# Optimization experiments

Measured on AMD Instinct MI355X. Metric: run time of the kernel, lower is better.

The kernel has to match this reference:

```python
import jax, jax.numpy as jnp
import numpy as np

EPS_GIN = 0.0      # GINConv eps (train_eps=False)
EPS_LN = 1e-5      # LayerNorm eps
EPS_GN = 1e-5      # GraphNorm eps


def _layer_norm(h, w, b):
    mu = jnp.mean(h, axis=-1, keepdims=True)
    var = jnp.mean(jnp.square(h - mu), axis=-1, keepdims=True)
    return (h - mu) * jax.lax.rsqrt(var + EPS_LN) * w + b


def setup_inputs() -> dict:
    key = jax.random.key(0)
    ks = jax.random.split(key, 6)
    N, E, C = 50000, 800000, 64
    x = jax.random.normal(ks[0], (N, C), dtype=jnp.float32)
    edge_index = jax.random.randint(ks[1], (2, E), 0, N, dtype=jnp.int64)
    W0 = jax.random.normal(ks[2], (C, C), dtype=jnp.float32) / np.sqrt(C)
    W1 = jax.random.normal(ks[3], (C, C), dtype=jnp.float32) / np.sqrt(C)
    ln0_w = jnp.ones((C,), jnp.float32); ln0_b = jnp.zeros((C,), jnp.float32)
    ln1_w = jnp.ones((C,), jnp.float32); ln1_b = jnp.zeros((C,), jnp.float32)
    # GraphNorm params
    gn_w = jnp.ones((C,), jnp.float32)
    gn_b = jnp.zeros((C,), jnp.float32)
    gn_alpha = jnp.ones((C,), jnp.float32)  # mean_scale
    return {"x": x, "edge_index": edge_index, "W0": W0, "ln0_w": ln0_w,
            "ln0_b": ln0_b, "W1": W1, "ln1_w": ln1_w, "ln1_b": ln1_b,
            "gn_w": gn_w, "gn_b": gn_b, "gn_alpha": gn_alpha}


def reference(x, edge_index, W0, ln0_w, ln0_b, W1, ln1_w, ln1_b, gn_w, gn_b, gn_alpha):
    N = x.shape[0]
    src, dst = edge_index[0], edge_index[1]
    # GINConv aggregation: sum of source-node features at each target node
    agg = jax.ops.segment_sum(x[src], dst, num_segments=N)  # [N, C]
    h = (1.0 + EPS_GIN) * x + agg
    # MLP: (Linear no-bias -> LayerNorm -> ReLU) x 2
    h = jax.nn.relu(_layer_norm(h @ W0.T, ln0_w, ln0_b))
    h = jax.nn.relu(_layer_norm(h @ W1.T, ln1_w, ln1_b))
    # GraphNorm over the single graph (all nodes)
    mean = jnp.mean(h, axis=0, keepdims=True)                # [1, C]
    out = h - gn_alpha * mean
    var = jnp.mean(jnp.square(out), axis=0, keepdims=True)   # [1, C]
    return gn_w * out * jax.lax.rsqrt(var + EPS_GN) + gn_b
```

## Files before the change

### kernel.cpp

```cpp
#include <hip/hip_runtime.h>
#include <hip/hip_fp16.h>
#include <stdint.h>

#define LN_EPS 1e-5f
#define GN_EPS 1e-5f

#define NSB 64
#define BE1 2048
#define CAP1R 88
#define RPC 22
#define CH2 18
#define NPB2 32
#define SLAB2 768
#define NFBA 2048
#define CAP2 768
#define NSLOT 16

__global__ __launch_bounds__(512) void k_sort1_half(
    const uint32_t* __restrict__ ew, int E, int PB1,
    const float* __restrict__ x, uint4* __restrict__ xh8, int n8,
    int* __restrict__ zbase, int nz, int* __restrict__ counts1,
    uint32_t* __restrict__ pairs1) {
  __shared__ int whist[8 * NSB];
  __shared__ int wbase[8 * NSB];
  __shared__ int wlcur[8 * NSB];
  __shared__ int binStart[NSB];
  __shared__ uint32_t stage[BE1];
  const int t = threadIdx.x;

  if (blockIdx.x >= PB1) {
    if (blockIdx.x == PB1) {
      for (int i = t; i < nz; i += 512) zbase[i] = 0;
    }
    int i = (blockIdx.x - PB1) * 512 + t;
    if (i >= n8) return;
    float4 a = *(const float4*)&x[i * 8];
    float4 b = *(const float4*)&x[i * 8 + 4];
    __half2 h0 = __floats2half2_rn(a.x, a.y);
    __half2 h1 = __floats2half2_rn(a.z, a.w);
    __half2 h2 = __floats2half2_rn(b.x, b.y);
    __half2 h3 = __floats2half2_rn(b.z, b.w);
    uint4 o;
    o.x = *(uint32_t*)&h0; o.y = *(uint32_t*)&h1;
    o.z = *(uint32_t*)&h2; o.w = *(uint32_t*)&h3;
    xh8[i] = o;
    return;
  }

  const int b = blockIdx.x;
  const int w = t >> 6;
  const int e0 = b * BE1;
  const int cnt = min(BE1, E - e0);

  uint32_t v = 0;
  if (t < cnt) v = ew[2 * (e0 + t) + 1];
  const int is32 = __syncthreads_or((int)(v != 0));

  whist[t] = 0;
  wlcur[t] = 0;
  __syncthreads();

  uint32_t myP[4];
  #pragma unroll
  for (int r = 0; r < 4; ++r) {
    int i = t + 512 * r;
    if (i < cnt) {
      long long e = e0 + i;
      int s, d;
      if (is32) {
        s = ((const int*)ew)[e];
        d = ((const int*)ew)[(long long)E + e];
      } else {
        s = (int)((const long long*)ew)[e];
        d = (int)((const long long*)ew)[(long long)E + e];
      }
      myP[r] = ((uint32_t)s << 16) | (uint32_t)d;
      atomicAdd(&whist[w * NSB + (d >> 10)], 1);
    }
  }
  __syncthreads();

  if (t < NSB) {
    int sum = 0;
    #pragma unroll
    for (int w2 = 0; w2 < 8; ++w2) {
      wbase[w2 * NSB + t] = sum;
      sum += whist[w2 * NSB + t];
    }
    int s = sum;
    #pragma unroll
    for (int d = 1; d < NSB; d <<= 1) {
      int o = __shfl_up(s, d, 64);
      if (t >= d) s += o;
    }
    binStart[t] = s - sum;
    counts1[t * PB1 + b] = sum;
  }
  __syncthreads();

  #pragma unroll
  for (int r = 0; r < 4; ++r) {
    int i = t + 512 * r;
    if (i < cnt) {
      int b2 = (int)(myP[r] & 0xFFFFu) >> 10;
      int p = binStart[b2] + wbase[w * NSB + b2] +
              atomicAdd(&wlcur[w * NSB + b2], 1);
      stage[p] = myP[r];
    }
  }
  __syncthreads();

  for (int i = t; i < cnt; i += 512) {
    uint32_t pr = stage[i];
    int sb = (int)(pr & 0xFFFFu) >> 10;
    int rel = i - binStart[sb];
    if (rel < CAP1R) pairs1[((size_t)b * NSB + sb) * CAP1R + rel] = pr;
  }
}

__global__ __launch_bounds__(512) void k_part2(
    const uint32_t* __restrict__ pairs1, const int* __restrict__ counts1,
    int PB1, int* cursors2, uint32_t* pairs2) {
  __shared__ int whist[8 * 32];
  __shared__ int wbase[8 * 32];
  __shared__ int wlcur[8 * 32];
  __shared__ int binStart[32], baseG[32];
  __shared__ int cLDS[RPC];
  __shared__ int totLDS;
  __shared__ uint32_t stage[BE1];
  const int t = threadIdx.x;
  const int w = t >> 6;
  const int sb = blockIdx.x / CH2;
  const int ch = blockIdx.x % CH2;
  const int r0 = ch * RPC;
  const int nr = min(RPC, PB1 - r0);

  if (t < 8 * 32) { whist[t] = 0; wlcur[t] = 0; }
  if (t < nr) cLDS[t] = counts1[sb * PB1 + r0 + t];
  __syncthreads();

  uint32_t myP[4];
  int myV[4];
  #pragma unroll
  for (int r = 0; r < 4; ++r) {
    int i = t + 512 * r;
    myV[r] = 0;
    if (i < nr * CAP1R) {
      int reg = i / CAP1R, idx = i % CAP1R;
      if (idx < cLDS[reg]) {
        myP[r] = pairs1[((size_t)(r0 + reg) * NSB + sb) * CAP1R + idx];
        myV[r] = 1;
        atomicAdd(&whist[(w << 5) + ((myP[r] >> 5) & 31)], 1);
      }
    }
  }
  __syncthreads();

  if (t < 32) {
    int sum = 0;
    #pragma unroll
    for (int w2 = 0; w2 < 8; ++w2) {
      wbase[(w2 << 5) + t] = sum;
      sum += whist[(w2 << 5) + t];
    }
    int s = sum;
    #pragma unroll
    for (int d = 1; d < 32; d <<= 1) {
      int o = __shfl_up(s, d, 32);
      if (t >= d) s += o;
    }
    binStart[t] = s - sum;
    baseG[t] = (sum > 0) ? atomicAdd(&cursors2[(sb << 5) + t], sum) : 0;
    if (t == 31) totLDS = s;
  }
  __syncthreads();

  #pragma unroll
  for (int r = 0; r < 4; ++r) {
    if (myV[r]) {
      int b2 = (int)(myP[r] >> 5) & 31;
      int p = binStart[b2] + wbase[(w << 5) + b2] +
              atomicAdd(&wlcur[(w << 5) + b2], 1);
      stage[p] = myP[r];
    }
  }
  __syncthreads();

  const int total = totLDS;
  for (int i = t; i < total; i += 512) {
    uint32_t pr = stage[i];
    int sub = (int)(pr >> 5) & 31;
    int o = baseG[sub] + (i - binStart[sub]);
    if (o < SLAB2) pairs2[(size_t)((sb << 5) + sub) * SLAB2 + o] = pr;
  }
}

__global__ __launch_bounds__(256, 8) void k_fused(
    const float4* __restrict__ x4, const uint4* __restrict__ xh8,
    const uint32_t* __restrict__ pairs, const int* __restrict__ cursors,
    const float* __restrict__ W0g, const float* __restrict__ ln0w,
    const float* __restrict__ ln0b, const float* __restrict__ W1g,
    const float* __restrict__ ln1w, const float* __restrict__ ln1b,
    float* __restrict__ out, int N, float* __restrict__ accum) {
  __shared__ __align__(16) float HYt[64 * 34];
  __shared__ __align__(16) float U[2048];
  int* hist = (int*)U;
  int* offs = hist + 32;
  int* lcur = offs + 32;
  int* list = lcur + 32;
  float* Wt = U;
  float* wsum = U;

  const int t = threadIdx.x;
  const int B = blockIdx.x;
  const int cnt = min(cursors[B], SLAB2);
  const uint32_t* pb = pairs + (size_t)B * SLAB2;
  const int node0 = B * NPB2;

  if (t < 32) hist[t] = 0;
  __syncthreads();

  for (int i = t; i < cnt; i += 256) atomicAdd(&hist[pb[i] & 31], 1);
  __syncthreads();

  if (t < 32) {
    int v = hist[t], s = v;
    #pragma unroll
    for (int d = 1; d < 32; d <<= 1) {
      int o = __shfl_up(s, d, 32);
      if (t >= d) s += o;
    }
    offs[t] = s - v;
    lcur[t] = s - v;
  }
  __syncthreads();

  for (int i = t; i < cnt; i += 256) {
    uint32_t p = pb[i];
    int pos = atomicAdd(&lcur[p & 31], 1);
    if (pos < CAP2) list[pos] = (int)(p >> 16);
  }
  __syncthreads();

  const int q8 = t & 7;
  const int nl = t >> 3;
  const int node = node0 + nl;
  float acc[8] = {};
  if (node < N) {
    float4 sa = x4[node * 16 + 2 * q8];
    float4 sb = x4[node * 16 + 2 * q8 + 1];
    acc[0] = sa.x; acc[1] = sa.y; acc[2] = sa.z; acc[3] = sa.w;
    acc[4] = sb.x; acc[5] = sb.y; acc[6] = sb.z; acc[7] = sb.w;
    int j = offs[nl];
    const int e = min(lcur[nl], CAP2);
    for (; j + 3 < e; j += 4) {
      uint4 v0 = xh8[list[j] * 8 + q8];
      uint4 v1 = xh8[list[j + 1] * 8 + q8];
      uint4 v2 = xh8[list[j + 2] * 8 + q8];
      uint4 v3 = xh8[list[j + 3] * 8 + q8];
      #pragma unroll
      for (int c = 0; c < 4; ++c) {
        uint32_t u0 = (&v0.x)[c], u1 = (&v1.x)[c];
        uint32_t u2 = (&v2.x)[c], u3 = (&v3.x)[c];
        float2 f0 = __half22float2(*(__half2*)&u0);
        float2 f1 = __half22float2(*(__half2*)&u1);
        float2 f2 = __half22float2(*(__half2*)&u2);
        float2 f3 = __half22float2(*(__half2*)&u3);
        acc[2 * c]     += (f0.x + f1.x) + (f2.x + f3.x);
        acc[2 * c + 1] += (f0.y + f1.y) + (f2.y + f3.y);
      }
    }
    for (; j < e; ++j) {
      uint4 v0 = xh8[list[j] * 8 + q8];
      #pragma unroll
      for (int c = 0; c < 4; ++c) {
        uint32_t u0 = (&v0.x)[c];
        float2 f0 = __half22float2(*(__half2*)&u0);
        acc[2 * c] += f0.x;
        acc[2 * c + 1] += f0.y;
      }
    }
  }
  __syncthreads();

  #pragma unroll
  for (int c = 0; c < 8; ++c) HYt[(8 * q8 + c) * 34 + nl] = acc[c];

  const int tx = t & 15;
  const int ty = t >> 4;
  const int wc = t & 63, ww = t >> 6;
  float a0[2][4] = {};

  #pragma unroll
  for (int half = 0; half < 2; ++half) {
    {
      #pragma unroll
      for (int r = 0; r < 2; ++r) {
        int k4 = ww * 4 + 16 * r;
        float4 v = *(const float4*)&W0g[wc * 64 + 32 * half + k4];
        Wt[(k4 + 0) * 64 + wc] = v.x; Wt[(k4 + 1) * 64 + wc] = v.y;
        Wt[(k4 + 2) * 64 + wc] = v.z; Wt[(k4 + 3) * 64 + wc] = v.w;
      }
    }
    __syncthreads();
    #pragma unroll 8
    for (int k = 0; k < 32; ++k) {
      float2 hh = *(const float2*)&HYt[(32 * half + k) * 34 + 2 * ty];
      float4 wv = *(const float4*)&Wt[k * 64 + 4 * tx];
      a0[0][0] += hh.x * wv.x; a0[0][1] += hh.x * wv.y;
      a0[0][2] += hh.x * wv.z; a0[0][3] += hh.x * wv.w;
      a0[1][0] += hh.y * wv.x; a0[1][1] += hh.y * wv.y;
      a0[1][2] += hh.y * wv.z; a0[1][3] += hh.y * wv.w;
    }
    __syncthreads();
  }

  {
    const float4 lw = *(const float4*)&ln0w[4 * tx];
    const float4 lb = *(const float4*)&ln0b[4 * tx];
    float y[2][4];
    #pragma unroll
    for (int j = 0; j < 2; ++j) {
      float s = a0[j][0] + a0[j][1] + a0[j][2] + a0[j][3];
      #pragma unroll
      for (int m = 1; m < 16; m <<= 1) s += __shfl_xor(s, m, 16);
      float mu = s * (1.f / 64.f);
      float d0 = a0[j][0] - mu, d1 = a0[j][1] - mu;
      float d2 = a0[j][2] - mu, d3 = a0[j][3] - mu;
      float vv = d0 * d0 + d1 * d1 + d2 * d2 + d3 * d3;
      #pragma unroll
      for (int m = 1; m < 16; m <<= 1) vv += __shfl_xor(vv, m, 16);
      float rs = rsqrtf(vv * (1.f / 64.f) + LN_EPS);
      y[j][0] = fmaxf(d0 * rs * lw.x + lb.x, 0.f);
      y[j][1] = fmaxf(d1 * rs * lw.y + lb.y, 0.f);
      y[j][2] = fmaxf(d2 * rs * lw.z + lb.z, 0.f);
      y[j][3] = fmaxf(d3 * rs * lw.w + lb.w, 0.f);
    }
    #pragma unroll
    for (int j = 0; j < 2; ++j) {
      int n = 2 * ty + j;
      HYt[(4 * tx + 0) * 34 + n] = y[j][0];
      HYt[(4 * tx + 1) * 34 + n] = y[j][1];
      HYt[(4 * tx + 2) * 34 + n] = y[j][2];
      HYt[(4 * tx + 3) * 34 + n] = y[j][3];
    }
  }
  __syncthreads();

  float a1[2][4] = {};
  #pragma unroll
  for (int half = 0; half < 2; ++half) {
    {
      #pragma unroll
      for (int r = 0; r < 2; ++r) {
        int k4 = ww * 4 + 16 * r;
        float4 v = *(const float4*)&W1g[wc * 64 + 32 * half + k4];
        Wt[(k4 + 0) * 64 + wc] = v.x; Wt[(k4 + 1) * 64 + wc] = v.y;
        Wt[(k4 + 2) * 64 + wc] = v.z; Wt[(k4 + 3) * 64 + wc] = v.w;
      }
    }
    __syncthreads();
    #pragma unroll 8
    for (int k = 0; k < 32; ++k) {
      float2 hh = *(const float2*)&HYt[(32 * half + k) * 34 + 2 * ty];
      float4 wv = *(const float4*)&Wt[k * 64 + 4 * tx];
      a1[0][0] += hh.x * wv.x; a1[0][1] += hh.x * wv.y;
      a1[0][2] += hh.x * wv.z; a1[0][3] += hh.x * wv.w;
      a1[1][0] += hh.y * wv.x; a1[1][1] += hh.y * wv.y;
      a1[1][2] += hh.y * wv.z; a1[1][3] += hh.y * wv.w;
    }
    __syncthreads();
  }

  const float4 lw = *(const float4*)&ln1w[4 * tx];
  const float4 lb = *(const float4*)&ln1b[4 * tx];
  float st1[4] = {0.f, 0.f, 0.f, 0.f}, st2[4] = {0.f, 0.f, 0.f, 0.f};
  #pragma unroll
  for (int j = 0; j < 2; ++j) {
    int nodej = node0 + 2 * ty + j;
    float s = a1[j][0] + a1[j][1] + a1[j][2] + a1[j][3];
    #pragma unroll
    for (int m = 1; m < 16; m <<= 1) s += __shfl_xor(s, m, 16);
    float mu = s * (1.f / 64.f);
    float d0 = a1[j][0] - mu, d1 = a1[j][1] - mu;
    float d2 = a1[j][2] - mu, d3 = a1[j][3] - mu;
    float vv = d0 * d0 + d1 * d1 + d2 * d2 + d3 * d3;
    #pragma unroll
    for (int m = 1; m < 16; m <<= 1) vv += __shfl_xor(vv, m, 16);
    float rs = rsqrtf(vv * (1.f / 64.f) + LN_EPS);
    float y0 = fmaxf(d0 * rs * lw.x + lb.x, 0.f);
    float y1 = fmaxf(d1 * rs * lw.y + lb.y, 0.f);
    float y2 = fmaxf(d2 * rs * lw.z + lb.z, 0.f);
    float y3 = fmaxf(d3 * rs * lw.w + lb.w, 0.f);
    if (nodej < N) {
      *(float4*)&out[(long long)nodej * 64 + 4 * tx] =
          make_float4(y0, y1, y2, y3);
      st1[0] += y0; st2[0] += y0 * y0;
      st1[1] += y1; st2[1] += y1 * y1;
      st1[2] += y2; st2[2] += y2 * y2;
      st1[3] += y3; st2[3] += y3 * y3;
    }
  }
  #pragma unroll
  for (int i = 0; i < 4; ++i) {
    st1[i] += __shfl_xor(st1[i], 16, 64); st1[i] += __shfl_xor(st1[i], 32, 64);
    st2[i] += __shfl_xor(st2[i], 16, 64); st2[i] += __shfl_xor(st2[i], 32, 64);
  }
  const int lane = t & 63, w = t >> 6;
  if (lane < 16) {
    #pragma unroll
    for (int i = 0; i < 4; ++i) {
      wsum[w * 128 + 4 * lane + i] = st1[i];
      wsum[w * 128 + 64 + 4 * lane + i] = st2[i];
    }
  }
  __syncthreads();
  if (t < 128) {
    float s = wsum[t] + wsum[128 + t] + wsum[256 + t] + wsum[384 + t];
    atomicAdd(&accum[(B & (NSLOT - 1)) * 128 + t], s);
  }
}

__global__ __launch_bounds__(256) void k_apply(
    const float4* __restrict__ h4, const float* __restrict__ accum,
    const float* __restrict__ alpha, const float* __restrict__ gnw,
    const float* __restrict__ gnb, float4* __restrict__ outp, int N) {
  __shared__ float cs[128];
  __shared__ float ab[128];
  const int t = threadIdx.x;
  if (t < 128) {
    float s = 0.f;
    #pragma unroll
    for (int sl = 0; sl < NSLOT; ++sl) s += accum[sl * 128 + t];
    cs[t] = s;
  }
  __syncthreads();
  if (t < 64) {
    float invN = 1.f / (float)N;
    float mu = cs[t] * invN;
    float e2 = cs[64 + t] * invN;
    float al = alpha[t];
    float var = e2 - 2.f * al * mu * mu + al * al * mu * mu;
    float a = gnw[t] * rsqrtf(var + GN_EPS);
    ab[t] = a;
    ab[64 + t] = gnb[t] - a * al * mu;
  }
  __syncthreads();
  int idx = blockIdx.x * 256 + t;
  if (idx < N * 16) {
    int q = idx & 15;
    float4 a = *(const float4*)&ab[q * 4];
    float4 b = *(const float4*)&ab[64 + q * 4];
    float4 h = h4[idx];
    outp[idx] = make_float4(a.x * h.x + b.x, a.y * h.y + b.y, a.z * h.z + b.z,
                            a.w * h.w + b.w);
  }
}

extern "C" void kernel_launch(void* const* d_in, const int* in_sizes, int n_in,
                              void* d_out, int out_size, void* d_ws,
                              size_t ws_size, hipStream_t stream) {
  const float* x    = (const float*)d_in[0];
  const void* edges = d_in[1];
  const float* W0   = (const float*)d_in[2];
  const float* ln0w = (const float*)d_in[3];
  const float* ln0b = (const float*)d_in[4];
  const float* W1   = (const float*)d_in[5];
  const float* ln1w = (const float*)d_in[6];
  const float* ln1b = (const float*)d_in[7];
  const float* gnw  = (const float*)d_in[8];
  const float* gnb  = (const float*)d_in[9];
  const float* gna  = (const float*)d_in[10];
  const int N = in_sizes[0] / 64;
  const int E = in_sizes[1] / 2;
  const int PB1 = (E + BE1 - 1) / BE1;
  const int HB  = (N * 8 + 511) / 512;
  const int nsb = (N + 1023) >> 10;
  const int nfb = nsb * 32;

  float* h         = (float*)d_ws;
  uint4* xh8       = (uint4*)(h + (size_t)N * 64);
  uint32_t* pairs1 = (uint32_t*)(xh8 + (size_t)N * 8);
  int* counts1     = (int*)(pairs1 + (size_t)PB1 * NSB * CAP1R);
  uint32_t* pairs2 = (uint32_t*)(counts1 + (size_t)NSB * PB1);
  int* cursors2    = (int*)(pairs2 + (size_t)NFBA * SLAB2);
  float* accum     = (float*)(cursors2 + NFBA);

  k_sort1_half<<<PB1 + HB, 512, 0, stream>>>(
      (const uint32_t*)edges, E, PB1, x, xh8, N * 8, cursors2,
      NFBA + NSLOT * 128, counts1, pairs1);
  k_part2<<<nsb * CH2, 512, 0, stream>>>(pairs1, counts1, PB1, cursors2,
                                         pairs2);
  k_fused<<<nfb, 256, 0, stream>>>((const float4*)x, xh8, pairs2, cursors2,
                                   W0, ln0w, ln0b, W1, ln1w, ln1b, h, N,
                                   accum);
  k_apply<<<(N * 16 + 255) / 256, 256, 0, stream>>>((const float4*)h, accum,
                                                    gna, gnw, gnb,
                                                    (float4*)d_out, N);
}
```

Measured before the change: 137.0 us.

## Use node-major HY layout and 4x4 register tiles on half the threads

```diff
diff --git a/kernel.cpp b/kernel.cpp
--- a/kernel.cpp
+++ b/kernel.cpp
@@ -195,14 +195,14 @@
   }
 }
 
-__global__ __launch_bounds__(256, 8) void k_fused(
+__global__ __launch_bounds__(256, 6) void k_fused(
     const float4* __restrict__ x4, const uint4* __restrict__ xh8,
     const uint32_t* __restrict__ pairs, const int* __restrict__ cursors,
     const float* __restrict__ W0g, const float* __restrict__ ln0w,
     const float* __restrict__ ln0b, const float* __restrict__ W1g,
     const float* __restrict__ ln1w, const float* __restrict__ ln1b,
     float* __restrict__ out, int N, float* __restrict__ accum) {
-  __shared__ __align__(16) float HYt[64 * 34];
+  __shared__ __align__(16) float HYt[32 * 68];
   __shared__ __align__(16) float U[2048];
   int* hist = (int*)U;
   int* offs = hist + 32;
@@ -283,13 +283,14 @@
   }
   __syncthreads();
 
-  #pragma unroll
-  for (int c = 0; c < 8; ++c) HYt[(8 * q8 + c) * 34 + nl] = acc[c];
+  *(float4*)&HYt[nl * 68 + 8 * q8] = make_float4(acc[0], acc[1], acc[2], acc[3]);
+  *(float4*)&HYt[nl * 68 + 8 * q8 + 4] = make_float4(acc[4], acc[5], acc[6], acc[7]);
 
   const int tx = t & 15;
-  const int ty = t >> 4;
+  const int ty8 = t >> 4;
   const int wc = t & 63, ww = t >> 6;
-  float a0[2][4] = {};
+  const bool act = t < 128;
+  float a0[4][4] = {};
 
   #pragma unroll
   for (int half = 0; half < 2; ++half) {
@@ -303,24 +304,37 @@
       }
     }
     __syncthreads();
-    #pragma unroll 8
-    for (int k = 0; k < 32; ++k) {
-      float2 hh = *(const float2*)&HYt[(32 * half + k) * 34 + 2 * ty];
-      float4 wv = *(const float4*)&Wt[k * 64 + 4 * tx];
-      a0[0][0] += hh.x * wv.x; a0[0][1] += hh.x * wv.y;
-      a0[0][2] += hh.x * wv.z; a0[0][3] += hh.x * wv.w;
-      a0[1][0] += hh.y * wv.x; a0[1][1] += hh.y * wv.y;
-      a0[1][2] += hh.y * wv.z; a0[1][3] += hh.y * wv.w;
+    if (act) {
+      #pragma unroll 2
+      for (int k4 = 0; k4 < 8; ++k4) {
+        float4 h0 = *(const float4*)&HYt[(4 * ty8 + 0) * 68 + 32 * half + 4 * k4];
+        float4 h1 = *(const float4*)&HYt[(4 * ty8 + 1) * 68 + 32 * half + 4 * k4];
+        float4 h2 = *(const float4*)&HYt[(4 * ty8 + 2) * 68 + 32 * half + 4 * k4];
+        float4 h3 = *(const float4*)&HYt[(4 * ty8 + 3) * 68 + 32 * half + 4 * k4];
+        #pragma unroll
+        for (int j = 0; j < 4; ++j) {
+          float4 wv = *(const float4*)&Wt[(4 * k4 + j) * 64 + 4 * tx];
+          float hj0 = (&h0.x)[j], hj1 = (&h1.x)[j];
+          float hj2 = (&h2.x)[j], hj3 = (&h3.x)[j];
+          a0[0][0] += hj0 * wv.x; a0[0][1] += hj0 * wv.y;
+          a0[0][2] += hj0 * wv.z; a0[0][3] += hj0 * wv.w;
+          a0[1][0] += hj1 * wv.x; a0[1][1] += hj1 * wv.y;
+          a0[1][2] += hj1 * wv.z; a0[1][3] += hj1 * wv.w;
+          a0[2][0] += hj2 * wv.x; a0[2][1] += hj2 * wv.y;
+          a0[2][2] += hj2 * wv.z; a0[2][3] += hj2 * wv.w;
+          a0[3][0] += hj3 * wv.x; a0[3][1] += hj3 * wv.y;
+          a0[3][2] += hj3 * wv.z; a0[3][3] += hj3 * wv.w;
+        }
+      }
     }
     __syncthreads();
   }
 
-  {
+  if (act) {
     const float4 lw = *(const float4*)&ln0w[4 * tx];
     const float4 lb = *(const float4*)&ln0b[4 * tx];
-    float y[2][4];
-    #pragma unroll
-    for (int j = 0; j < 2; ++j) {
+    #pragma unroll
+    for (int j = 0; j < 4; ++j) {
       float s = a0[j][0] + a0[j][1] + a0[j][2] + a0[j][3];
       #pragma unroll
       for (int m = 1; m < 16; m <<= 1) s += __shfl_xor(s, m, 16);
@@ -331,23 +345,13 @@
       #pragma unroll
       for (int m = 1; m < 16; m <<= 1) vv += __shfl_xor(vv, m, 16);
       float rs = rsqrtf(vv * (1.f / 64.f) + LN_EPS);
-      y[j][0] = fmaxf(d0 * rs * lw.x + lb.x, 0.f);
-      y[j][1] = fmaxf(d1 * rs * lw.y + lb.y, 0.f);
-      y[j][2] = fmaxf(d2 * rs * lw.z + lb.z, 0.f);
-      y[j][3] = fmaxf(d3 * rs * lw.w + lb.w, 0.f);
-    }
-    #pragma unroll
-    for (int j = 0; j < 2; ++j) {
-      int n = 2 * ty + j;
-      HYt[(4 * tx + 0) * 34 + n] = y[j][0];
-      HYt[(4 * tx + 1) * 34 + n] = y[j][1];
-      HYt[(4 * tx + 2) * 34 + n] = y[j][2];
-      HYt[(4 * tx + 3) * 34 + n] = y[j][3];
-    }
-  }
-  __syncthreads();
-
-  float a1[2][4] = {};
+      *(float4*)&HYt[(4 * ty8 + j) * 68 + 4 * tx] = make_float4(
+          fmaxf(d0 * rs * lw.x + lb.x, 0.f), fmaxf(d1 * rs * lw.y + lb.y, 0.f),
+          fmaxf(d2 * rs * lw.z + lb.z, 0.f), fmaxf(d3 * rs * lw.w + lb.w, 0.f));
+    }
+  }
+
+  float a1[4][4] = {};
   #pragma unroll
   for (int half = 0; half < 2; ++half) {
     {
@@ -360,54 +364,72 @@
       }
     }
     __syncthreads();
-    #pragma unroll 8
-    for (int k = 0; k < 32; ++k) {
-      float2 hh = *(const float2*)&HYt[(32 * half + k) * 34 + 2 * ty];
-      float4 wv = *(const float4*)&Wt[k * 64 + 4 * tx];
-      a1[0][0] += hh.x * wv.x; a1[0][1] += hh.x * wv.y;
-      a1[0][2] += hh.x * wv.z; a1[0][3] += hh.x * wv.w;
-      a1[1][0] += hh.y * wv.x; a1[1][1] += hh.y * wv.y;
-      a1[1][2] += hh.y * wv.z; a1[1][3] += hh.y * wv.w;
+    if (act) {
+      #pragma unroll 2
+      for (int k4 = 0; k4 < 8; ++k4) {
+        float4 h0 = *(const float4*)&HYt[(4 * ty8 + 0) * 68 + 32 * half + 4 * k4];
+        float4 h1 = *(const float4*)&HYt[(4 * ty8 + 1) * 68 + 32 * half + 4 * k4];
+        float4 h2 = *(const float4*)&HYt[(4 * ty8 + 2) * 68 + 32 * half + 4 * k4];
+        float4 h3 = *(const float4*)&HYt[(4 * ty8 + 3) * 68 + 32 * half + 4 * k4];
+        #pragma unroll
+        for (int j = 0; j < 4; ++j) {
+          float4 wv = *(const float4*)&Wt[(4 * k4 + j) * 64 + 4 * tx];
+          float hj0 = (&h0.x)[j], hj1 = (&h1.x)[j];
+          float hj2 = (&h2.x)[j], hj3 = (&h3.x)[j];
+          a1[0][0] += hj0 * wv.x; a1[0][1] += hj0 * wv.y;
+          a1[0][2] += hj0 * wv.z; a1[0][3] += hj0 * wv.w;
+          a1[1][0] += hj1 * wv.x; a1[1][1] += hj1 * wv.y;
+          a1[1][2] += hj1 * wv.z; a1[1][3] += hj1 * wv.w;
+          a1[2][0] += hj2 * wv.x; a1[2][1] += hj2 * wv.y;
+          a1[2][2] += hj2 * wv.z; a1[2][3] += hj2 * wv.w;
+          a1[3][0] += hj3 * wv.x; a1[3][1] += hj3 * wv.y;
+          a1[3][2] += hj3 * wv.z; a1[3][3] += hj3 * wv.w;
+        }
+      }
     }
     __syncthreads();
   }
 
-  const float4 lw = *(const float4*)&ln1w[4 * tx];
-  const float4 lb = *(const float4*)&ln1b[4 * tx];
   float st1[4] = {0.f, 0.f, 0.f, 0.f}, st2[4] = {0.f, 0.f, 0.f, 0.f};
-  #pragma unroll
-  for (int j = 0; j < 2; ++j) {
-    int nodej = node0 + 2 * ty + j;
-    float s = a1[j][0] + a1[j][1] + a1[j][2] + a1[j][3];
-    #pragma unroll
-    for (int m = 1; m < 16; m <<= 1) s += __shfl_xor(s, m, 16);
-    float mu = s * (1.f / 64.f);
-    float d0 = a1[j][0] - mu, d1 = a1[j][1] - mu;
-    float d2 = a1[j][2] - mu, d3 = a1[j][3] - mu;
-    float vv = d0 * d0 + d1 * d1 + d2 * d2 + d3 * d3;
-    #pragma unroll
-    for (int m = 1; m < 16; m <<= 1) vv += __shfl_xor(vv, m, 16);
-    float rs = rsqrtf(vv * (1.f / 64.f) + LN_EPS);
-    float y0 = fmaxf(d0 * rs * lw.x + lb.x, 0.f);
-    float y1 = fmaxf(d1 * rs * lw.y + lb.y, 0.f);
-    float y2 = fmaxf(d2 * rs * lw.z + lb.z, 0.f);
-    float y3 = fmaxf(d3 * rs * lw.w + lb.w, 0.f);
-    if (nodej < N) {
-      *(float4*)&out[(long long)nodej * 64 + 4 * tx] =
-          make_float4(y0, y1, y2, y3);
-      st1[0] += y0; st2[0] += y0 * y0;
-      st1[1] += y1; st2[1] += y1 * y1;
-      st1[2] += y2; st2[2] += y2 * y2;
-      st1[3] += y3; st2[3] += y3 * y3;
-    }
-  }
-  #pragma unroll
-  for (int i = 0; i < 4; ++i) {
-    st1[i] += __shfl_xor(st1[i], 16, 64); st1[i] += __shfl_xor(st1[i], 32, 64);
-    st2[i] += __shfl_xor(st2[i], 16, 64); st2[i] += __shfl_xor(st2[i], 32, 64);
+  if (act) {
+    const float4 lw = *(const float4*)&ln1w[4 * tx];
+    const float4 lb = *(const float4*)&ln1b[4 * tx];
+    #pragma unroll
+    for (int j = 0; j < 4; ++j) {
+      int nodej = node0 + 4 * ty8 + j;
+      float s = a1[j][0] + a1[j][1] + a1[j][2] + a1[j][3];
+      #pragma unroll
+      for (int m = 1; m < 16; m <<= 1) s += __shfl_xor(s, m, 16);
+      float mu = s * (1.f / 64.f);
+      float d0 = a1[j][0] - mu, d1 = a1[j][1] - mu;
+      float d2 = a1[j][2] - mu, d3 = a1[j][3] - mu;
+      float vv = d0 * d0 + d1 * d1 + d2 * d2 + d3 * d3;
+      #pragma unroll
+      for (int m = 1; m < 16; m <<= 1) vv += __shfl_xor(vv, m, 16);
+      float rs = rsqrtf(vv * (1.f / 64.f) + LN_EPS);
+      float y0 = fmaxf(d0 * rs * lw.x + lb.x, 0.f);
+      float y1 = fmaxf(d1 * rs * lw.y + lb.y, 0.f);
+      float y2 = fmaxf(d2 * rs * lw.z + lb.z, 0.f);
+      float y3 = fmaxf(d3 * rs * lw.w + lb.w, 0.f);
+      if (nodej < N) {
+        *(float4*)&out[(long long)nodej * 64 + 4 * tx] =
+            make_float4(y0, y1, y2, y3);
+        st1[0] += y0; st2[0] += y0 * y0;
+        st1[1] += y1; st2[1] += y1 * y1;
+        st1[2] += y2; st2[2] += y2 * y2;
+        st1[3] += y3; st2[3] += y3 * y3;
+      }
+    }
+    #pragma unroll
+    for (int i = 0; i < 4; ++i) {
+      st1[i] += __shfl_xor(st1[i], 16, 64);
+      st1[i] += __shfl_xor(st1[i], 32, 64);
+      st2[i] += __shfl_xor(st2[i], 16, 64);
+      st2[i] += __shfl_xor(st2[i], 32, 64);
+    }
   }
   const int lane = t & 63, w = t >> 6;
-  if (lane < 16) {
+  if (act && lane < 16) {
     #pragma unroll
     for (int i = 0; i < 4; ++i) {
       wsum[w * 128 + 4 * lane + i] = st1[i];
@@ -416,7 +438,7 @@
   }
   __syncthreads();
   if (t < 128) {
-    float s = wsum[t] + wsum[128 + t] + wsum[256 + t] + wsum[384 + t];
+    float s = wsum[t] + wsum[128 + t];
     atomicAdd(&accum[(B & (NSLOT - 1)) * 128 + t], s);
   }
 }
```

Result: slower. 142.1 us (+3.7%).

## Use fp16 MFMA for both MLP matmuls with pre-converted fp16 weights

Applied to the files above, without the earlier changes.

```diff
diff --git a/kernel.cpp b/kernel.cpp
--- a/kernel.cpp
+++ b/kernel.cpp
@@ -16,11 +16,16 @@
 #define CAP2 768
 #define NSLOT 16
 
+typedef _Float16 f16x8 __attribute__((ext_vector_type(8)));
+typedef _Float16 f16x4 __attribute__((ext_vector_type(4)));
+typedef float f32x4 __attribute__((ext_vector_type(4)));
+
 __global__ __launch_bounds__(512) void k_sort1_half(
     const uint32_t* __restrict__ ew, int E, int PB1,
     const float* __restrict__ x, uint4* __restrict__ xh8, int n8,
-    int* __restrict__ zbase, int nz, int* __restrict__ counts1,
-    uint32_t* __restrict__ pairs1) {
+    int* __restrict__ zbase, int nz, const float* __restrict__ W0g,
+    const float* __restrict__ W1g, _Float16* __restrict__ whg,
+    int* __restrict__ counts1, uint32_t* __restrict__ pairs1) {
   __shared__ int whist[8 * NSB];
   __shared__ int wbase[8 * NSB];
   __shared__ int wlcur[8 * NSB];
@@ -31,6 +36,8 @@
   if (blockIdx.x >= PB1) {
     if (blockIdx.x == PB1) {
       for (int i = t; i < nz; i += 512) zbase[i] = 0;
+      for (int i = t; i < 8192; i += 512)
+        whg[i] = (_Float16)((i < 4096) ? W0g[i] : W1g[i - 4096]);
     }
     int i = (blockIdx.x - PB1) * 512 + t;
     if (i >= n8) return;
@@ -198,18 +205,18 @@
 __global__ __launch_bounds__(256, 8) void k_fused(
     const float4* __restrict__ x4, const uint4* __restrict__ xh8,
     const uint32_t* __restrict__ pairs, const int* __restrict__ cursors,
-    const float* __restrict__ W0g, const float* __restrict__ ln0w,
-    const float* __restrict__ ln0b, const float* __restrict__ W1g,
-    const float* __restrict__ ln1w, const float* __restrict__ ln1b,
-    float* __restrict__ out, int N, float* __restrict__ accum) {
-  __shared__ __align__(16) float HYt[64 * 34];
-  __shared__ __align__(16) float U[2048];
-  int* hist = (int*)U;
-  int* offs = hist + 32;
-  int* lcur = offs + 32;
-  int* list = lcur + 32;
-  float* Wt = U;
-  float* wsum = U;
+    const _Float16* __restrict__ whg, const float* __restrict__ ln0w,
+    const float* __restrict__ ln0b, const float* __restrict__ ln1w,
+    const float* __restrict__ ln1b, float* __restrict__ out, int N,
+    float* __restrict__ accum) {
+  __shared__ __align__(16) _Float16 Hh[32 * 72];
+  __shared__ __align__(16) float Yf[32 * 68];
+  __shared__ __align__(16) int Us[896];
+  int* hist = Us;
+  int* offs = Us + 32;
+  int* lcur = Us + 64;
+  int* list = Us + 96;
+  float* wsum = (float*)Us;
 
   const int t = threadIdx.x;
   const int B = blockIdx.x;
@@ -281,96 +288,84 @@
       }
     }
   }
-  __syncthreads();
-
-  #pragma unroll
-  for (int c = 0; c < 8; ++c) HYt[(8 * q8 + c) * 34 + nl] = acc[c];
-
-  const int tx = t & 15;
-  const int ty = t >> 4;
-  const int wc = t & 63, ww = t >> 6;
-  float a0[2][4] = {};
-
-  #pragma unroll
-  for (int half = 0; half < 2; ++half) {
-    {
-      #pragma unroll
-      for (int r = 0; r < 2; ++r) {
-        int k4 = ww * 4 + 16 * r;
-        float4 v = *(const float4*)&W0g[wc * 64 + 32 * half + k4];
-        Wt[(k4 + 0) * 64 + wc] = v.x; Wt[(k4 + 1) * 64 + wc] = v.y;
-        Wt[(k4 + 2) * 64 + wc] = v.z; Wt[(k4 + 3) * 64 + wc] = v.w;
-      }
-    }
-    __syncthreads();
-    #pragma unroll 8
-    for (int k = 0; k < 32; ++k) {
-      float2 hh = *(const float2*)&HYt[(32 * half + k) * 34 + 2 * ty];
-      float4 wv = *(const float4*)&Wt[k * 64 + 4 * tx];
-      a0[0][0] += hh.x * wv.x; a0[0][1] += hh.x * wv.y;
-      a0[0][2] += hh.x * wv.z; a0[0][3] += hh.x * wv.w;
-      a0[1][0] += hh.y * wv.x; a0[1][1] += hh.y * wv.y;
-      a0[1][2] += hh.y * wv.z; a0[1][3] += hh.y * wv.w;
-    }
-    __syncthreads();
-  }
+
+  {
+    f16x8 hv;
+    #pragma unroll
+    for (int c = 0; c < 8; ++c) hv[c] = (_Float16)acc[c];
+    *(f16x8*)&Hh[nl * 72 + 8 * q8] = hv;
+  }
+  __syncthreads();
+
+  const int l = t & 63, wv = t >> 6;
+  const int tx = t & 15, ty = t >> 4;
+  const int ar = l & 15, ak = (l >> 4) * 8;
+
+  {
+    f16x8 a00 = *(f16x8*)&Hh[ar * 72 + ak];
+    f16x8 a01 = *(f16x8*)&Hh[ar * 72 + 32 + ak];
+    f16x8 a10 = *(f16x8*)&Hh[(ar + 16) * 72 + ak];
+    f16x8 a11 = *(f16x8*)&Hh[(ar + 16) * 72 + 32 + ak];
+    f16x8 b0 = *(const f16x8*)&whg[(16 * wv + ar) * 64 + ak];
+    f16x8 b1 = *(const f16x8*)&whg[(16 * wv + ar) * 64 + 32 + ak];
+    f32x4 d0 = {0.f, 0.f, 0.f, 0.f}, d1 = {0.f, 0.f, 0.f, 0.f};
+    d0 = __builtin_amdgcn_mfma_f32_16x16x32_f16(a00, b0, d0, 0, 0, 0);
+    d0 = __builtin_amdgcn_mfma_f32_16x16x32_f16(a01, b1, d0, 0, 0, 0);
+    d1 = __builtin_amdgcn_mfma_f32_16x16x32_f16(a10, b0, d1, 0, 0, 0);
+    d1 = __builtin_amdgcn_mfma_f32_16x16x32_f16(a11, b1, d1, 0, 0, 0);
+    #pragma unroll
+    for (int r = 0; r < 4; ++r) {
+      Yf[((l >> 4) * 4 + r) * 68 + 16 * wv + ar] = d0[r];
+      Yf[((l >> 4) * 4 + r + 16) * 68 + 16 * wv + ar] = d1[r];
+    }
+  }
+  __syncthreads();
 
   {
     const float4 lw = *(const float4*)&ln0w[4 * tx];
     const float4 lb = *(const float4*)&ln0b[4 * tx];
-    float y[2][4];
     #pragma unroll
     for (int j = 0; j < 2; ++j) {
-      float s = a0[j][0] + a0[j][1] + a0[j][2] + a0[j][3];
+      float4 v = *(const float4*)&Yf[(2 * ty + j) * 68 + 4 * tx];
+      float s = v.x + v.y + v.z + v.w;
       #pragma unroll
       for (int m = 1; m < 16; m <<= 1) s += __shfl_xor(s, m, 16);
       float mu = s * (1.f / 64.f);
-      float d0 = a0[j][0] - mu, d1 = a0[j][1] - mu;
-      float d2 = a0[j][2] - mu, d3 = a0[j][3] - mu;
+      float d0 = v.x - mu, d1 = v.y - mu, d2 = v.z - mu, d3 = v.w - mu;
       float vv = d0 * d0 + d1 * d1 + d2 * d2 + d3 * d3;
       #pragma unroll
       for (int m = 1; m < 16; m <<= 1) vv += __shfl_xor(vv, m, 16);
       float rs = rsqrtf(vv * (1.f / 64.f) + LN_EPS);
-      y[j][0] = fmaxf(d0 * rs * lw.x + lb.x, 0.f);
-      y[j][1] = fmaxf(d1 * rs * lw.y + lb.y, 0.f);
-      y[j][2] = fmaxf(d2 * rs * lw.z + lb.z, 0.f);
-      y[j][3] = fmaxf(d3 * rs * lw.w + lb.w, 0.f);
-    }
-    #pragma unroll
-    for (int j = 0; j < 2; ++j) {
-      int n = 2 * ty + j;
-      HYt[(4 * tx + 0) * 34 + n] = y[j][0];
-      HYt[(4 * tx + 1) * 34 + n] = y[j][1];
-      HYt[(4 * tx + 2) * 34 + n] = y[j][2];
-      HYt[(4 * tx + 3) * 34 + n] = y[j][3];
-    }
-  }
-  __syncthreads();
-
-  float a1[2][4] = {};
-  #pragma unroll
-  for (int half = 0; half < 2; ++half) {
-    {
-      #pragma unroll
-      for (int r = 0; r < 2; ++r) {
-        int k4 = ww * 4 + 16 * r;
-        float4 v = *(const float4*)&W1g[wc * 64 + 32 * half + k4];
-        Wt[(k4 + 0) * 64 + wc] = v.x; Wt[(k4 + 1) * 64 + wc] = v.y;
-        Wt[(k4 + 2) * 64 + wc] = v.z; Wt[(k4 + 3) * 64 + wc] = v.w;
-      }
-    }
+      f16x4 yv;
+      yv[0] = (_Float16)fmaxf(d0 * rs * lw.x + lb.x, 0.f);
+      yv[1] = (_Float16)fmaxf(d1 * rs * lw.y + lb.y, 0.f);
+      yv[2] = (_Float16)fmaxf(d2 * rs * lw.z + lb.z, 0.f);
+      yv[3] = (_Float16)fmaxf(d3 * rs * lw.w + lb.w, 0.f);
+      *(f16x4*)&Hh[(2 * ty + j) * 72 + 4 * tx] = yv;
+    }
+  }
+  __syncthreads();
+
+  {
+    f16x8 a00 = *(f16x8*)&Hh[ar * 72 + ak];
+    f16x8 a01 = *(f16x8*)&Hh[ar * 72 + 32 + ak];
+    f16x8 a10 = *(f16x8*)&Hh[(ar + 16) * 72 + ak];
+    f16x8 a11 = *(f16x8*)&Hh[(ar + 16) * 72 + 32 + ak];
+    f16x8 b0 = *(const f16x8*)&whg[4096 + (16 * wv + ar) * 64 + ak];
+    f16x8 b1 = *(const f16x8*)&whg[4096 + (16 * wv + ar) * 64 + 32 + ak];
+    f32x4 d0 = {0.f, 0.f, 0.f, 0.f}, d1 = {0.f, 0.f, 0.f, 0.f};
+    d0 = __builtin_amdgcn_mfma_f32_16x16x32_f16(a00, b0, d0, 0, 0, 0);
+    d0 = __builtin_amdgcn_mfma_f32_16x16x32_f16(a01, b1, d0, 0, 0, 0);
+    d1 = __builtin_amdgcn_mfma_f32_16x16x32_f16(a10, b0, d1, 0, 0, 0);
+    d1 = __builtin_amdgcn_mfma_f32_16x16x32_f16(a11, b1, d1, 0, 0, 0);
     __syncthreads();
-    #pragma unroll 8
-    for (int k = 0; k < 32; ++k) {
-      float2 hh = *(const float2*)&HYt[(32 * half + k) * 34 + 2 * ty];
-      float4 wv = *(const float4*)&Wt[k * 64 + 4 * tx];
-      a1[0][0] += hh.x * wv.x; a1[0][1] += hh.x * wv.y;
-      a1[0][2] += hh.x * wv.z; a1[0][3] += hh.x * wv.w;
-      a1[1][0] += hh.y * wv.x; a1[1][1] += hh.y * wv.y;
-      a1[1][2] += hh.y * wv.z; a1[1][3] += hh.y * wv.w;
-    }
-    __syncthreads();
-  }
+    #pragma unroll
+    for (int r = 0; r < 4; ++r) {
+      Yf[((l >> 4) * 4 + r) * 68 + 16 * wv + ar] = d0[r];
+      Yf[((l >> 4) * 4 + r + 16) * 68 + 16 * wv + ar] = d1[r];
+    }
+  }
+  __syncthreads();
 
   const float4 lw = *(const float4*)&ln1w[4 * tx];
   const float4 lb = *(const float4*)&ln1b[4 * tx];
@@ -378,12 +373,12 @@
   #pragma unroll
   for (int j = 0; j < 2; ++j) {
     int nodej = node0 + 2 * ty + j;
-    float s = a1[j][0] + a1[j][1] + a1[j][2] + a1[j][3];
+    float4 v = *(const float4*)&Yf[(2 * ty + j) * 68 + 4 * tx];
+    float s = v.x + v.y + v.z + v.w;
     #pragma unroll
     for (int m = 1; m < 16; m <<= 1) s += __shfl_xor(s, m, 16);
     float mu = s * (1.f / 64.f);
-    float d0 = a1[j][0] - mu, d1 = a1[j][1] - mu;
-    float d2 = a1[j][2] - mu, d3 = a1[j][3] - mu;
+    float d0 = v.x - mu, d1 = v.y - mu, d2 = v.z - mu, d3 = v.w - mu;
     float vv = d0 * d0 + d1 * d1 + d2 * d2 + d3 * d3;
     #pragma unroll
     for (int m = 1; m < 16; m <<= 1) vv += __shfl_xor(vv, m, 16);
@@ -406,6 +401,7 @@
     st1[i] += __shfl_xor(st1[i], 16, 64); st1[i] += __shfl_xor(st1[i], 32, 64);
     st2[i] += __shfl_xor(st2[i], 16, 64); st2[i] += __shfl_xor(st2[i], 32, 64);
   }
+  __syncthreads();
   const int lane = t & 63, w = t >> 6;
   if (lane < 16) {
     #pragma unroll
@@ -485,15 +481,15 @@
   uint32_t* pairs2 = (uint32_t*)(counts1 + (size_t)NSB * PB1);
   int* cursors2    = (int*)(pairs2 + (size_t)NFBA * SLAB2);
   float* accum     = (float*)(cursors2 + NFBA);
+  _Float16* whg    = (_Float16*)(accum + NSLOT * 128);
 
   k_sort1_half<<<PB1 + HB, 512, 0, stream>>>(
       (const uint32_t*)edges, E, PB1, x, xh8, N * 8, cursors2,
-      NFBA + NSLOT * 128, counts1, pairs1);
+      NFBA + NSLOT * 128, W0, W1, whg, counts1, pairs1);
   k_part2<<<nsb * CH2, 512, 0, stream>>>(pairs1, counts1, PB1, cursors2,
                                          pairs2);
   k_fused<<<nfb, 256, 0, stream>>>((const float4*)x, xh8, pairs2, cursors2,
-                                   W0, ln0w, ln0b, W1, ln1w, ln1b, h, N,
-                                   accum);
+                                   whg, ln0w, ln0b, ln1w, ln1b, h, N, accum);
   k_apply<<<(N * 16 + 255) / 256, 256, 0, stream>>>((const float4*)h, accum,
                                                     gna, gnw, gnb,
                                                     (float4*)d_out, N);
```

Measured after the change: 123.4 us. -9.9%, faster.
